# Kernel tuning notes

Measured on AMD Instinct MI355X. Metric: run time of the kernel, lower is better.

Reference implementation:

```python
import jax, jax.numpy as jnp
import numpy as np

G = 8           # graphs
NBG = 1024      # blocks per graph
APB = 4         # atoms per block
NC = 1          # coord channels
HID = 512
ES = 64
K = 9
L = 3
NLVL = 50
NB = G * NBG
NU = NB * APB
NUM_BLOCK, NUM_ATOM, NUM_POS = 25, 16, 16
BIG = 1e9


def _cumsum_ids(seg_lengths, n):
    # faithful to torch: zeros, mark segment starts via cumsum(lengths)[:-1], cumsum
    ids = jnp.zeros((n,), jnp.int32).at[jnp.cumsum(seg_lengths)[:-1]].set(1)
    return jnp.cumsum(ids)


def setup_inputs() -> dict:
    key = jax.random.key(0)
    ks = jax.random.split(key, 18)
    s = 0.02
    return {
        'Z': 3.0 * jax.random.normal(ks[0], (NU, NC, 3), jnp.float32),
        'B': jax.random.randint(ks[1], (NB,), 0, NUM_BLOCK),
        'A': jax.random.randint(ks[2], (NU,), 0, NUM_ATOM),
        'atom_positions': jax.random.randint(ks[3], (NU,), 0, NUM_POS),
        'block_lengths': jnp.full((NB,), APB, jnp.int32),
        'lengths': jnp.full((G,), NBG, jnp.int32),
        'segment_ids': jax.random.randint(ks[4], (NB,), 0, 2),
        'noise': jax.random.normal(ks[5], (NU, NC, 3), jnp.float32),
        'noise_level': jax.random.randint(ks[6], (G,), 0, NLVL),
        'sigmas': jnp.asarray(np.exp(np.linspace(np.log(10.0), np.log(0.01), NLVL)), jnp.float32),
        'atom_emb': s * jax.random.normal(ks[7], (NUM_ATOM, HID), jnp.float32),
        'pos_emb': s * jax.random.normal(ks[8], (NUM_POS, HID), jnp.float32),
        'block_emb': s * jax.random.normal(ks[9], (NUM_BLOCK, HID), jnp.float32),
        'edge_emb': s * jax.random.normal(ks[10], (2, ES), jnp.float32),
        'Wm': s * jax.random.normal(ks[11], (L, HID, HID), jnp.float32),
        'We': s * jax.random.normal(ks[12], (L, ES, HID), jnp.float32),
        'Wu': s * jax.random.normal(ks[13], (L, HID, HID), jnp.float32),
        'wz': s * jax.random.normal(ks[14], (L, HID), jnp.float32),
        'W1': s * jax.random.normal(ks[15], (HID, HID), jnp.float32),
        'b1': jnp.zeros((HID,), jnp.float32),
        'W2': s * jax.random.normal(ks[16], (HID, 1), jnp.float32),
    }


def _forward(Z, B, A, atom_positions, block_lengths, lengths, segment_ids,
             noise, noise_level, sigmas, atom_emb, pos_emb, block_emb, edge_emb,
             Wm, We, Wu, wz, W1, b1, W2):
    nb, nu, g = B.shape[0], A.shape[0], lengths.shape[0]
    nbg, apb = nb // g, nu // nb
    batch_id = _cumsum_ids(lengths, nb)        # [Nb]
    block_id = _cumsum_ids(block_lengths, nu)  # [Nu]

    # perturb: Z + noise * sigma[noise_level[graph]]
    used = sigmas[noise_level][batch_id][block_id]          # [Nu]
    Zp = Z + noise * used[:, None, None]                    # [Nu, NC, 3]

    # block embedding: atom + position + block-type
    H0 = atom_emb[A] + pos_emb[atom_positions] + block_emb[B][block_id]  # [Nu, H]

    # edges: fully connect -> split intra/inter by segment -> knn by min atom-pair distance
    xa = Zp.reshape(g, nbg * apb * NC, 3)
    sq = jnp.sum(xa * xa, axis=-1)
    d2 = sq[:, :, None] + sq[:, None, :] - 2.0 * jnp.einsum('gnd,gmd->gnm', xa, xa)
    D = d2.reshape(g, nbg, apb * NC, nbg, apb * NC).min(axis=(2, 4))     # [g, nbg, nbg]
    seg = segment_ids.reshape(g, nbg)
    same = seg[:, :, None] == seg[:, None, :]
    eye = jnp.eye(nbg, dtype=bool)[None]
    _, idx_intra = jax.lax.top_k(-jnp.where(same & ~eye, D, BIG), K)     # [g, nbg, K]
    _, idx_inter = jax.lax.top_k(-jnp.where(~same, D, BIG), K)
    off = (jnp.arange(g, dtype=jnp.int32) * nbg)[:, None, None]
    dst_loc = jnp.broadcast_to(jnp.arange(nbg, dtype=jnp.int32)[None, :, None] + off, (g, nbg, K))
    src = jnp.concatenate([(idx_intra + off).reshape(-1), (idx_inter + off).reshape(-1)])
    dst = jnp.concatenate([dst_loc.reshape(-1), dst_loc.reshape(-1)])
    eattr = edge_emb[jnp.concatenate([jnp.zeros(g * nbg * K, jnp.int32), jnp.ones(g * nbg * K, jnp.int32)])]

    # encoder (GET surrogate): block-level equivariant message passing
    h = jax.ops.segment_sum(H0, block_id, num_segments=nb) / apb                    # [Nb, H]
    Zb0 = jax.ops.segment_sum(Zp.mean(axis=1), block_id, num_segments=nb) / apb    # [Nb, 3]
    Zb = Zb0
    for l in range(Wm.shape[0]):
        m = jax.nn.silu((h[src] + h[dst]) @ Wm[l] + eattr @ We[l])                  # [E, H]
        h = h + jax.nn.silu(jax.ops.segment_sum(m, dst, num_segments=nb) @ Wu[l])
        coef = jnp.tanh(m @ wz[l])                                                  # [E]
        Zb = Zb + jax.ops.segment_sum((Zb[src] - Zb[dst]) * coef[:, None], dst, num_segments=nb) / (2 * K)
    pred_Z = Zp + (Zb - Zb0)[block_id][:, None, :]
    unit_repr = H0 + h[block_id]
    block_repr = h
    graph_repr = jax.ops.segment_sum(h, batch_id, num_segments=g)

    # energy head: SiLU -> Linear -> SiLU -> Linear(no bias), summed per graph
    e = jax.nn.silu(jax.nn.silu(block_repr) @ W1 + b1) @ W2                         # [Nb, 1]
    pred_energy = jax.ops.segment_sum(e[:, 0], batch_id, num_segments=g)            # [g]

    pred_noise = pred_Z - Zp
    per_unit = jnp.sum((pred_noise - noise) ** 2, axis=(-1, -2))                    # [Nu]
    nl = jax.ops.segment_sum(per_unit, batch_id[block_id], num_segments=g)
    loss = 0.5 * nl.mean()
    return pred_energy, pred_noise, unit_repr, block_repr, graph_repr, loss


def reference(Z, B, A, atom_positions, block_lengths, lengths, segment_ids,
              noise, noise_level, sigmas, atom_emb, pos_emb, block_emb, edge_emb,
              Wm, We, Wu, wz, W1, b1, W2):
    return _forward(Z, B, A, atom_positions, block_lengths, lengths, segment_ids,
                    noise, noise_level, sigmas, atom_emb, pos_emb, block_emb, edge_emb,
                    Wm, We, Wu, wz, W1, b1, W2)
```

## Files before the change

kernel.cpp:

```cpp
#include <hip/hip_runtime.h>
#include <hip/hip_bf16.h>

typedef __bf16 bf16;
typedef __bf16 bf16x2 __attribute__((ext_vector_type(2)));
typedef __bf16 bf16x8 __attribute__((ext_vector_type(8)));
typedef float floatx4 __attribute__((ext_vector_type(4)));

#define NB_ 8192
#define NU_ 32768

__device__ __forceinline__ float silu_f(float x) {
    float e = __expf(-x);
    return x * __builtin_amdgcn_rcpf(1.0f + e);
}

__device__ __forceinline__ float2 unpack_bf2(unsigned v) {
    float2 r;
    r.x = __uint_as_float(v << 16);
    r.y = __uint_as_float(v & 0xFFFF0000u);
    return r;
}

__device__ __forceinline__ void gll16(const bf16* g, bf16* l) {
    __builtin_amdgcn_global_load_lds((const __attribute__((address_space(1))) void*)g,
                                     (__attribute__((address_space(3))) void*)l, 16, 0, 0);
}

__global__ __launch_bounds__(256) void init_kernel(
    const float* __restrict__ Z, const float* __restrict__ noise,
    const int* __restrict__ nl, const float* __restrict__ sig,
    const int* __restrict__ Aarr, const int* __restrict__ posa, const int* __restrict__ Barr,
    const float* __restrict__ atom_emb, const float* __restrict__ pos_emb,
    const float* __restrict__ block_emb,
    const float* __restrict__ edge_emb, const float* __restrict__ We,
    const float* __restrict__ Wm, const float* __restrict__ Wu, const float* __restrict__ W1,
    float* __restrict__ Zp, float* __restrict__ Zb0, float* __restrict__ Zb,
    float* __restrict__ hf, bf16* __restrict__ hb,
    bf16* __restrict__ WmT, bf16* __restrict__ WuT, bf16* __restrict__ W1T,
    float* __restrict__ ebias,
    float* __restrict__ out_gr, float* __restrict__ out_e, float* __restrict__ out_loss)
{
    __shared__ float zsh[12];
    __shared__ float tile[32][33];
    int bid = blockIdx.x, tid = threadIdx.x;
    if (bid < 8192) {
        int b = bid, g = b >> 10;
        if (tid < 12) {
            float sg = sig[nl[g]];
            int idx = b*12 + tid;
            float zp = Z[idx] + noise[idx]*sg;
            Zp[idx] = zp;
            zsh[tid] = zp;
        }
        __syncthreads();
        if (tid < 3) {
            float v = 0.25f*(zsh[tid] + zsh[3+tid] + zsh[6+tid] + zsh[9+tid]);
            Zb0[b*3+tid] = v; Zb[b*3+tid] = v;
        }
        int ai[4], pi[4];
        #pragma unroll
        for (int a = 0; a < 4; a++) { ai[a] = Aarr[b*4+a]*512; pi[a] = posa[b*4+a]*512; }
        int bb = Barr[b]*512;
        #pragma unroll
        for (int cc = 0; cc < 2; cc++) {
            int c = tid + cc*256;
            float s = 0.0f;
            #pragma unroll
            for (int a = 0; a < 4; a++) s += atom_emb[ai[a]+c] + pos_emb[pi[a]+c];
            s = 0.25f*s + block_emb[bb+c];
            hf[(size_t)b*512+c] = s;
            hb[(size_t)b*512+c] = (bf16)s;
        }
        return;
    }
    bid -= 8192;
    if (bid < 1792) {
        int z = bid >> 8, rem = bid & 255;
        int bx = rem & 15, by = rem >> 4;
        int tx = tid & 31, ty = tid >> 5;
        const float* src; bf16* dst;
        if (z < 3)      { src = Wm + (size_t)z*262144;     dst = WmT + (size_t)z*262144; }
        else if (z < 6) { src = Wu + (size_t)(z-3)*262144; dst = WuT + (size_t)(z-3)*262144; }
        else            { src = W1;                        dst = W1T; }
        #pragma unroll
        for (int i = 0; i < 32; i += 8)
            tile[ty+i][tx] = src[(size_t)(by*32+ty+i)*512 + bx*32+tx];
        __syncthreads();
        #pragma unroll
        for (int i = 0; i < 32; i += 8)
            dst[(size_t)(bx*32+ty+i)*512 + by*32+tx] = (bf16)tile[tx][ty+i];
        return;
    }
    bid -= 1792;
    if (bid < 12) {
        int gid = bid*256 + tid;
        int l = gid >> 10, t = (gid >> 9) & 1, c = gid & 511;
        float s = 0.0f;
        #pragma unroll 8
        for (int e = 0; e < 64; e++)
            s += edge_emb[t*64 + e] * We[(size_t)(l*64 + e)*512 + c];
        ebias[gid] = s;
        return;
    }
    bid -= 12;
    int k = bid*256 + tid;
    if (k < 4096) out_gr[k] = 0.0f;
    else if (k < 4104) out_e[k-4096] = 0.0f;
    else if (k == 4104) out_loss[0] = 0.0f;
}

__device__ void knn_body(int kb, const float* __restrict__ Zp, const int* __restrict__ seg,
                         int* __restrict__ nbr) {
    int wid = threadIdx.x >> 6;
    int lane = threadIdx.x & 63;
    int r = ((kb & 7) << 10) + ((kb >> 3) << 2) + wid;
    int g = r >> 10;
    int il = r & 1023;
    int base = g << 10;
    int segr = seg[r];
    float za[4][3];
    #pragma unroll
    for (int a = 0; a < 4; a++)
        #pragma unroll
        for (int d = 0; d < 3; d++)
            za[a][d] = Zp[r*12 + a*3 + d];
    float dist[16];
    unsigned smask = 0;
    #pragma unroll
    for (int t = 0; t < 16; t++) {
        int jb = base + t*64 + lane;
        const float4* p = (const float4*)(Zp + (size_t)jb*12);
        float4 v0 = p[0], v1 = p[1], v2 = p[2];
        float bx[4] = {v0.x, v0.w, v1.z, v2.y};
        float by[4] = {v0.y, v1.x, v1.w, v2.z};
        float bz[4] = {v0.z, v1.y, v2.x, v2.w};
        float dm = 3.0e38f;
        #pragma unroll
        for (int a = 0; a < 4; a++) {
            #pragma unroll
            for (int bq = 0; bq < 4; bq++) {
                float dx = za[a][0]-bx[bq], dy = za[a][1]-by[bq], dz = za[a][2]-bz[bq];
                dm = fminf(dm, dx*dx + dy*dy + dz*dz);
            }
        }
        dist[t] = dm;
        if (seg[jb] == segr) smask |= (1u << t);
    }
    const float INF = 3.0e38f;
    for (int phase = 0; phase < 2; phase++) {
        float wd[16];
        #pragma unroll
        for (int t = 0; t < 16; t++) {
            bool ok = (phase == 0) ? (((smask >> t) & 1u) && (t*64 + lane != il))
                                   : (!((smask >> t) & 1u));
            wd[t] = ok ? dist[t] : INF;
        }
        for (int it = 0; it < 9; it++) {
            float bd = wd[0]; int bt = 0;
            #pragma unroll
            for (int t = 1; t < 16; t++) { if (wd[t] < bd) { bd = wd[t]; bt = t; } }
            float mv = bd;
            #pragma unroll
            for (int off = 32; off >= 1; off >>= 1) mv = fminf(mv, __shfl_xor(mv, off, 64));
            unsigned long long msk = __ballot(bd == mv);
            int wl = __ffsll(msk) - 1;
            int wt = __shfl(bt, wl, 64);
            if (lane == 0) nbr[r*18 + phase*9 + it] = base + wt*64 + wl;
            bool amwin = (lane == wl);
            #pragma unroll
            for (int t = 0; t < 16; t++) if (amwin && t == wt) wd[t] = INF;
        }
    }
}

template<int PIPE>
__device__ void gemm_body(const bf16* __restrict__ A, const bf16* __restrict__ BT,
                          bf16* __restrict__ Pb, float* __restrict__ hf,
                          bf16* __restrict__ hb, bf16* __restrict__ shp,
                          const float* __restrict__ b1, const float* __restrict__ W2,
                          float* __restrict__ out_e,
                          float* __restrict__ Zb, const float* __restrict__ zacc,
                          int mode, int bid)
{
    constexpr int NBUF = PIPE ? 3 : 1;
    __shared__ alignas(16) bf16 sA[NBUF*128*32];
    __shared__ alignas(16) bf16 sB[NBUF*64*32];
    int mt = bid & 63, nt = bid >> 6;
    int m0 = mt*128, n0 = nt*64;
    int tid = threadIdx.x, lane = tid & 63, w = tid >> 6;
    int wm = w & 1, wn = w >> 1;
    int lm = lane & 15, q = lane >> 4;

    int pA0 = w*128 + lane, pA1 = pA0 + 64, pB = w*64 + lane;
    int rA0 = pA0 >> 2, qA0 = (pA0 & 3) ^ ((rA0 >> 1) & 3);
    int rA1 = pA1 >> 2, qA1 = (pA1 & 3) ^ ((rA1 >> 1) & 3);
    int rB  = pB  >> 2, qB  = (pB  & 3) ^ ((rB  >> 1) & 3);
    const bf16* gA0 = A  + (size_t)(m0 + rA0)*512 + qA0*8;
    const bf16* gA1 = A  + (size_t)(m0 + rA1)*512 + qA1*8;
    const bf16* gB  = BT + (size_t)(n0 + rB )*512 + qB*8;
    int dA0 = (w*128)*8, dA1 = (w*128 + 64)*8, dB = (w*64)*8;

    int swq = (q ^ ((lm >> 1) & 3)) * 8;
    int offA[4], offB[2];
    #pragma unroll
    for (int tm = 0; tm < 4; tm++) offA[tm] = (wm*64 + tm*16 + lm)*32 + swq;
    #pragma unroll
    for (int tn = 0; tn < 2; tn++) offB[tn] = (wn*32 + tn*16 + lm)*32 + swq;

    floatx4 zv = {0.0f, 0.0f, 0.0f, 0.0f};
    floatx4 acc[4][2];
    #pragma unroll
    for (int i = 0; i < 4; i++)
        #pragma unroll
        for (int j = 0; j < 2; j++) acc[i][j] = zv;

    if constexpr (PIPE == 0) {
        for (int k0 = 0; k0 < 512; k0 += 32) {
            gll16(gA0 + k0, sA + dA0);
            gll16(gA1 + k0, sA + dA1);
            gll16(gB  + k0, sB + dB);
            __syncthreads();
            bf16x8 af[4], bfr[2];
            #pragma unroll
            for (int tm = 0; tm < 4; tm++) af[tm] = *(const bf16x8*)(sA + offA[tm]);
            #pragma unroll
            for (int tn = 0; tn < 2; tn++) bfr[tn] = *(const bf16x8*)(sB + offB[tn]);
            #pragma unroll
            for (int tm = 0; tm < 4; tm++)
                #pragma unroll
                for (int tn = 0; tn < 2; tn++)
                    acc[tm][tn] = __builtin_amdgcn_mfma_f32_16x16x32_bf16(af[tm], bfr[tn], acc[tm][tn], 0, 0, 0);
            __syncthreads();
        }
    } else {
        gll16(gA0,      sA + dA0);
        gll16(gA1,      sA + dA1);
        gll16(gB,       sB + dB);
        gll16(gA0 + 32, sA + 4096 + dA0);
        gll16(gA1 + 32, sA + 4096 + dA1);
        gll16(gB  + 32, sB + 2048 + dB);
        #pragma unroll
        for (int t = 0; t < 16; t++) {
            const int cur = t % 3;
            if (t < 14) {
                const int k0 = (t + 2) * 32;
                const int nb = (t + 2) % 3;
                gll16(gA0 + k0, sA + nb*4096 + dA0);
                gll16(gA1 + k0, sA + nb*4096 + dA1);
                gll16(gB  + k0, sB + nb*2048 + dB);
                asm volatile("s_waitcnt vmcnt(6)" ::: "memory");
            } else if (t == 14) {
                asm volatile("s_waitcnt vmcnt(3)" ::: "memory");
            } else {
                asm volatile("s_waitcnt vmcnt(0)" ::: "memory");
            }
            __builtin_amdgcn_s_barrier();
            asm volatile("" ::: "memory");
            const bf16* a_ = sA + cur*4096;
            const bf16* b_ = sB + cur*2048;
            bf16x8 af[4], bfr[2];
            #pragma unroll
            for (int tm = 0; tm < 4; tm++) af[tm] = *(const bf16x8*)(a_ + offA[tm]);
            #pragma unroll
            for (int tn = 0; tn < 2; tn++) bfr[tn] = *(const bf16x8*)(b_ + offB[tn]);
            #pragma unroll
            for (int tm = 0; tm < 4; tm++)
                #pragma unroll
                for (int tn = 0; tn < 2; tn++)
                    acc[tm][tn] = __builtin_amdgcn_mfma_f32_16x16x32_bf16(af[tm], bfr[tn], acc[tm][tn], 0, 0, 0);
            asm volatile("" ::: "memory");
            __builtin_amdgcn_s_barrier();
        }
    }

    if (mode == 1 && nt == 0) {
        int o = m0*3 + tid;
        Zb[o] += zacc[o] * (1.0f/18.0f);
        if (tid < 128) {
            int o2 = m0*3 + 256 + tid;
            Zb[o2] += zacc[o2] * (1.0f/18.0f);
        }
    }

    if (mode == 2) {
        float esum = 0.0f;
        #pragma unroll
        for (int tn = 0; tn < 2; tn++) {
            int col = n0 + wn*32 + tn*16 + lm;
            float bb = b1[col];
            float w2 = W2[col];
            #pragma unroll
            for (int tm = 0; tm < 4; tm++)
                #pragma unroll
                for (int rr = 0; rr < 4; rr++)
                    esum += silu_f(acc[tm][tn][rr] + bb) * w2;
        }
        #pragma unroll
        for (int off = 32; off >= 1; off >>= 1) esum += __shfl_xor(esum, off, 64);
        __shared__ float ered[4];
        if (lane == 0) ered[w] = esum;
        __syncthreads();
        if (tid == 0) {
            float tot = ered[0] + ered[1] + ered[2] + ered[3];
            atomicAdd(&out_e[m0 >> 10], tot);
        }
        return;
    }
    #pragma unroll
    for (int tm = 0; tm < 4; tm++) {
        #pragma unroll
        for (int tn = 0; tn < 2; tn++) {
            #pragma unroll
            for (int rr = 0; rr < 4; rr++) {
                int row = m0 + wm*64 + tm*16 + q*4 + rr;
                int col = n0 + wn*32 + tn*16 + lm;
                size_t o = (size_t)row*512 + col;
                float v = acc[tm][tn][rr];
                if (mode == 0) {
                    Pb[o] = (bf16)v;
                } else {
                    float nh = hf[o] + silu_f(v);
                    hf[o] = nh;
                    hb[o] = (bf16)nh;
                    if (shp) shp[o] = (bf16)silu_f(nh);
                }
            }
        }
    }
}

__global__ __launch_bounds__(256) void gemm_kernel(const bf16* __restrict__ A, const bf16* __restrict__ BT,
                                                   bf16* __restrict__ Pb, float* __restrict__ hf,
                                                   bf16* __restrict__ hb, bf16* __restrict__ shp,
                                                   const float* __restrict__ b1, const float* __restrict__ W2,
                                                   float* __restrict__ out_e,
                                                   float* __restrict__ Zb, const float* __restrict__ zacc,
                                                   int mode) {
    gemm_body<1>(A, BT, Pb, hf, hb, shp, b1, W2, out_e, Zb, zacc, mode, blockIdx.x);
}

__global__ __launch_bounds__(256) void knn_pgemm0_kernel(const bf16* __restrict__ hb,
                                                         const bf16* __restrict__ WmT0,
                                                         bf16* __restrict__ Pb,
                                                         const float* __restrict__ Zp,
                                                         const int* __restrict__ seg,
                                                         int* __restrict__ nbr) {
    if (blockIdx.x < 512)
        gemm_body<0>(hb, WmT0, Pb, nullptr, nullptr, nullptr, nullptr, nullptr, nullptr,
                     nullptr, nullptr, 0, blockIdx.x);
    else
        knn_body(blockIdx.x - 512, Zp, seg, nbr);
}

__global__ __launch_bounds__(256) void edge_kernel(const bf16* __restrict__ Pb, const float* __restrict__ ebias,
                                                   const float* __restrict__ wz, const float* __restrict__ Zb,
                                                   const int* __restrict__ nbr, bf16* __restrict__ msum,
                                                   float* __restrict__ zacc) {
    int bid = blockIdx.x, tid = threadIdx.x;
    int b = ((bid & 7) << 10) | (bid >> 3);
    int c0 = 2*tid;
    int lane = tid & 63, wid = tid >> 6;
    __shared__ int srcs[18];
    __shared__ float red[18][4];
    __shared__ float term[18][3];
    if (tid < 18) srcs[tid] = nbr[b*18 + tid];
    __syncthreads();
    float2 pd  = unpack_bf2(*(const unsigned*)(Pb + (size_t)b*512 + c0));
    float2 eb0 = *(const float2*)(ebias + c0);
    float2 eb1 = *(const float2*)(ebias + 512 + c0);
    float2 w   = *(const float2*)(wz + c0);
    float ms0 = 0.0f, ms1 = 0.0f;
    float pdot[18];
    #pragma unroll
    for (int e = 0; e < 18; e++) {
        int s = srcs[e];
        float2 pv = unpack_bf2(*(const unsigned*)(Pb + (size_t)s*512 + c0));
        float ba = (e < 9) ? eb0.x : eb1.x;
        float bb = (e < 9) ? eb0.y : eb1.y;
        float m0 = silu_f(pv.x + pd.x + ba);
        float m1 = silu_f(pv.y + pd.y + bb);
        ms0 += m0; ms1 += m1;
        pdot[e] = m0*w.x + m1*w.y;
    }
    bf16x2 mp = { (bf16)ms0, (bf16)ms1 };
    *(bf16x2*)(msum + (size_t)b*512 + c0) = mp;
    #pragma unroll
    for (int e = 0; e < 18; e++) {
        float v = pdot[e];
        #pragma unroll
        for (int off = 32; off >= 1; off >>= 1) v += __shfl_xor(v, off, 64);
        if (lane == 0) red[e][wid] = v;
    }
    __syncthreads();
    if (tid < 18) {
        float dot = red[tid][0] + red[tid][1] + red[tid][2] + red[tid][3];
        float coef = tanhf(dot);
        int s = srcs[tid];
        #pragma unroll
        for (int d = 0; d < 3; d++)
            term[tid][d] = (Zb[s*3 + d] - Zb[b*3 + d]) * coef;
    }
    __syncthreads();
    if (tid < 3) {
        float s = 0.0f;
        #pragma unroll
        for (int e = 0; e < 18; e++) s += term[e][tid];
        zacc[b*3 + tid] = s;
    }
}

__global__ __launch_bounds__(256) void finalize_kernel(const float* __restrict__ hf, float* __restrict__ out_gr,
                                                       const float* __restrict__ Zb, const float* __restrict__ Zb0,
                                                       const float* __restrict__ noise,
                                                       float* __restrict__ out_pn, float* __restrict__ out_loss) {
    __shared__ float red[256];
    int bid = blockIdx.x, tid = threadIdx.x;
    if (bid < 128) {
        int u = bid*256 + tid;
        int b = u >> 2;
        float per = 0.0f;
        #pragma unroll
        for (int d = 0; d < 3; d++) {
            float dv = Zb[b*3+d] - Zb0[b*3+d];
            out_pn[u*3+d] = dv;
            float e = dv - noise[u*3+d];
            per += e*e;
        }
        red[tid] = per; __syncthreads();
        for (int st = 128; st > 0; st >>= 1) {
            if (tid < st) red[tid] += red[tid+st];
            __syncthreads();
        }
        if (tid == 0) atomicAdd(out_loss, red[0] * (1.0f/16.0f));
        return;
    }
    int pid = bid - 128;
    int g = pid >> 5;
    int rc = (pid >> 1) & 15;
    int ch = pid & 1;
    int c = ch*256 + tid;
    int b0 = (g << 10) + rc*64;
    float s = 0.0f;
    for (int i = 0; i < 64; i++) s += hf[(size_t)(b0+i)*512 + c];
    atomicAdd(&out_gr[g*512 + c], s);
}

__global__ __launch_bounds__(256) void unitrepr_kernel(const int* __restrict__ Aarr, const int* __restrict__ posa,
                                                       const int* __restrict__ Barr,
                                                       const float* __restrict__ atom_emb, const float* __restrict__ pos_emb,
                                                       const float* __restrict__ block_emb,
                                                       const float* __restrict__ hf, float* __restrict__ out_ur) {
    int gid = blockIdx.x*256 + threadIdx.x;
    int u = gid >> 7, c = (gid & 127) << 2, b = u >> 2;
    float4 va = *(const float4*)(atom_emb + (size_t)Aarr[u]*512 + c);
    float4 vp = *(const float4*)(pos_emb + (size_t)posa[u]*512 + c);
    float4 vb = *(const float4*)(block_emb + (size_t)Barr[b]*512 + c);
    float4 vh = *(const float4*)(hf + (size_t)b*512 + c);
    float4 o;
    o.x = va.x + vp.x + vb.x + vh.x;
    o.y = va.y + vp.y + vb.y + vh.y;
    o.z = va.z + vp.z + vb.z + vh.z;
    o.w = va.w + vp.w + vb.w + vh.w;
    *(float4*)(out_ur + (size_t)u*512 + c) = o;
}

extern "C" void kernel_launch(void* const* d_in, const int* in_sizes, int n_in,
                              void* d_out, int out_size, void* d_ws, size_t ws_size,
                              hipStream_t stream) {
    const float* Z         = (const float*)d_in[0];
    const int*   B         = (const int*)d_in[1];
    const int*   A         = (const int*)d_in[2];
    const int*   ap        = (const int*)d_in[3];
    const int*   seg       = (const int*)d_in[6];
    const float* noise     = (const float*)d_in[7];
    const int*   nl        = (const int*)d_in[8];
    const float* sig       = (const float*)d_in[9];
    const float* atom_emb  = (const float*)d_in[10];
    const float* pos_emb   = (const float*)d_in[11];
    const float* block_emb = (const float*)d_in[12];
    const float* edge_emb  = (const float*)d_in[13];
    const float* Wm        = (const float*)d_in[14];
    const float* We        = (const float*)d_in[15];
    const float* Wu        = (const float*)d_in[16];
    const float* wz        = (const float*)d_in[17];
    const float* W1        = (const float*)d_in[18];
    const float* b1        = (const float*)d_in[19];
    const float* W2        = (const float*)d_in[20];
    (void)in_sizes; (void)n_in; (void)d_ws; (void)ws_size; (void)out_size;

    float* out = (float*)d_out;
    const size_t o1 = 8, o2 = 98312, o3 = 16875528, o4 = 21069832, o5 = 21073928;
    float* out_e    = out;
    float* out_pn   = out + o1;
    float* out_ur   = out + o2;
    float* hf       = out + o3;
    float* out_gr   = out + o4;
    float* out_loss = out + o5;

    char* arena = (char*)(out + o2);
    bf16*  Pb   = (bf16*)(arena);
    bf16*  msum = (bf16*)(arena + 16777216);
    bf16*  sh   = (bf16*)(arena + 25165824);
    bf16*  hb   = (bf16*)(arena + 33554432);
    float* Zp   = (float*)(arena + 41943040);
    float* Zb0  = (float*)(arena + 42336256);
    float* Zb   = (float*)(arena + 42434560);
    float* zacc = (float*)(arena + 42532864);
    int*   nbr  = (int*)  (arena + 42631168);
    bf16*  WmT  = (bf16*) (arena + 43220992);
    bf16*  WuT  = (bf16*) (arena + 44793856);
    bf16*  W1T  = (bf16*) (arena + 46366720);
    float* ebias= (float*)(arena + 46891008);

    init_kernel<<<8192 + 1792 + 12 + 17, 256, 0, stream>>>(
        Z, noise, nl, sig, A, ap, B, atom_emb, pos_emb, block_emb,
        edge_emb, We, Wm, Wu, W1,
        Zp, Zb0, Zb, hf, hb, WmT, WuT, W1T, ebias, out_gr, out_e, out_loss);

    knn_pgemm0_kernel<<<512 + 2048, 256, 0, stream>>>(hb, WmT, Pb, Zp, seg, nbr);

    for (int l = 0; l < 3; l++) {
        if (l > 0)
            gemm_kernel<<<512, 256, 0, stream>>>(hb, WmT + (size_t)l*262144, Pb,
                                                 nullptr, nullptr, nullptr, nullptr, nullptr, nullptr,
                                                 nullptr, nullptr, 0);
        edge_kernel<<<8192, 256, 0, stream>>>(Pb, ebias + l*1024, wz + l*512, Zb, nbr, msum, zacc);
        gemm_kernel<<<512, 256, 0, stream>>>(msum, WuT + (size_t)l*262144, nullptr,
                                             hf, hb, (l == 2) ? sh : nullptr, nullptr, nullptr, nullptr,
                                             Zb, zacc, 1);
    }
    gemm_kernel<<<512, 256, 0, stream>>>(sh, W1T, nullptr, nullptr, nullptr, nullptr,
                                         b1, W2, out_e, nullptr, nullptr, 2);
    finalize_kernel<<<384, 256, 0, stream>>>(hf, out_gr, Zb, Zb0, noise, out_pn, out_loss);
    unitrepr_kernel<<<16384, 256, 0, stream>>>(A, ap, B, atom_emb, pos_emb, block_emb, hf, out_ur);
}
```

Baseline: 482.8 us.

## Fuse finalize into last update GEMM and move weight prep into kNN launch

```diff
diff --git a/kernel.cpp b/kernel.cpp
--- a/kernel.cpp
+++ b/kernel.cpp
@@ -5,9 +5,7 @@
 typedef __bf16 bf16x2 __attribute__((ext_vector_type(2)));
 typedef __bf16 bf16x8 __attribute__((ext_vector_type(8)));
 typedef float floatx4 __attribute__((ext_vector_type(4)));
-
-#define NB_ 8192
-#define NU_ 32768
+typedef float floatx2 __attribute__((ext_vector_type(2)));
 
 __device__ __forceinline__ float silu_f(float x) {
     float e = __expf(-x);
@@ -32,13 +30,10 @@
     const int* __restrict__ Aarr, const int* __restrict__ posa, const int* __restrict__ Barr,
     const float* __restrict__ atom_emb, const float* __restrict__ pos_emb,
     const float* __restrict__ block_emb,
-    const float* __restrict__ edge_emb, const float* __restrict__ We,
-    const float* __restrict__ Wm, const float* __restrict__ Wu, const float* __restrict__ W1,
+    const float* __restrict__ Wm,
     float* __restrict__ Zp, float* __restrict__ Zb0, float* __restrict__ Zb,
     float* __restrict__ hf, bf16* __restrict__ hb,
-    bf16* __restrict__ WmT, bf16* __restrict__ WuT, bf16* __restrict__ W1T,
-    float* __restrict__ ebias,
-    float* __restrict__ out_gr, float* __restrict__ out_e, float* __restrict__ out_loss)
+    bf16* __restrict__ WmT)
 {
     __shared__ float zsh[12];
     __shared__ float tile[32][33];
@@ -73,40 +68,16 @@
         }
         return;
     }
-    bid -= 8192;
-    if (bid < 1792) {
-        int z = bid >> 8, rem = bid & 255;
-        int bx = rem & 15, by = rem >> 4;
-        int tx = tid & 31, ty = tid >> 5;
-        const float* src; bf16* dst;
-        if (z < 3)      { src = Wm + (size_t)z*262144;     dst = WmT + (size_t)z*262144; }
-        else if (z < 6) { src = Wu + (size_t)(z-3)*262144; dst = WuT + (size_t)(z-3)*262144; }
-        else            { src = W1;                        dst = W1T; }
-        #pragma unroll
-        for (int i = 0; i < 32; i += 8)
-            tile[ty+i][tx] = src[(size_t)(by*32+ty+i)*512 + bx*32+tx];
-        __syncthreads();
-        #pragma unroll
-        for (int i = 0; i < 32; i += 8)
-            dst[(size_t)(bx*32+ty+i)*512 + by*32+tx] = (bf16)tile[tx][ty+i];
-        return;
-    }
-    bid -= 1792;
-    if (bid < 12) {
-        int gid = bid*256 + tid;
-        int l = gid >> 10, t = (gid >> 9) & 1, c = gid & 511;
-        float s = 0.0f;
-        #pragma unroll 8
-        for (int e = 0; e < 64; e++)
-            s += edge_emb[t*64 + e] * We[(size_t)(l*64 + e)*512 + c];
-        ebias[gid] = s;
-        return;
-    }
-    bid -= 12;
-    int k = bid*256 + tid;
-    if (k < 4096) out_gr[k] = 0.0f;
-    else if (k < 4104) out_e[k-4096] = 0.0f;
-    else if (k == 4104) out_loss[0] = 0.0f;
+    int rem = bid - 8192;
+    int bx = rem & 15, by = rem >> 4;
+    int tx = tid & 31, ty = tid >> 5;
+    #pragma unroll
+    for (int i = 0; i < 32; i += 8)
+        tile[ty+i][tx] = Wm[(size_t)(by*32+ty+i)*512 + bx*32+tx];
+    __syncthreads();
+    #pragma unroll
+    for (int i = 0; i < 32; i += 8)
+        WmT[(size_t)(bx*32+ty+i)*512 + by*32+tx] = (bf16)tile[tx][ty+i];
 }
 
 __device__ void knn_body(int kb, const float* __restrict__ Zp, const int* __restrict__ seg,
@@ -124,6 +95,13 @@
         #pragma unroll
         for (int d = 0; d < 3; d++)
             za[a][d] = Zp[r*12 + a*3 + d];
+    floatx2 ax[4], ay[4], az[4];
+    #pragma unroll
+    for (int a = 0; a < 4; a++) {
+        ax[a] = (floatx2){za[a][0], za[a][0]};
+        ay[a] = (floatx2){za[a][1], za[a][1]};
+        az[a] = (floatx2){za[a][2], za[a][2]};
+    }
     float dist[16];
     unsigned smask = 0;
     #pragma unroll
@@ -131,19 +109,19 @@
         int jb = base + t*64 + lane;
         const float4* p = (const float4*)(Zp + (size_t)jb*12);
         float4 v0 = p[0], v1 = p[1], v2 = p[2];
-        float bx[4] = {v0.x, v0.w, v1.z, v2.y};
-        float by[4] = {v0.y, v1.x, v1.w, v2.z};
-        float bz[4] = {v0.z, v1.y, v2.x, v2.w};
-        float dm = 3.0e38f;
+        floatx2 bx0 = {v0.x, v0.w}, by0 = {v0.y, v1.x}, bz0 = {v0.z, v1.y};
+        floatx2 bx1 = {v1.z, v2.y}, by1 = {v1.w, v2.z}, bz1 = {v2.x, v2.w};
+        floatx2 mn = {3.0e38f, 3.0e38f};
         #pragma unroll
         for (int a = 0; a < 4; a++) {
-            #pragma unroll
-            for (int bq = 0; bq < 4; bq++) {
-                float dx = za[a][0]-bx[bq], dy = za[a][1]-by[bq], dz = za[a][2]-bz[bq];
-                dm = fminf(dm, dx*dx + dy*dy + dz*dz);
-            }
-        }
-        dist[t] = dm;
+            floatx2 dx = ax[a] - bx0, dy = ay[a] - by0, dz = az[a] - bz0;
+            floatx2 dd = dx*dx + dy*dy + dz*dz;
+            mn.x = fminf(mn.x, dd.x); mn.y = fminf(mn.y, dd.y);
+            dx = ax[a] - bx1; dy = ay[a] - by1; dz = az[a] - bz1;
+            dd = dx*dx + dy*dy + dz*dz;
+            mn.x = fminf(mn.x, dd.x); mn.y = fminf(mn.y, dd.y);
+        }
+        dist[t] = fminf(mn.x, mn.y);
         if (seg[jb] == segr) smask |= (1u << t);
     }
     const float INF = 3.0e38f;
@@ -180,11 +158,17 @@
                           const float* __restrict__ b1, const float* __restrict__ W2,
                           float* __restrict__ out_e,
                           float* __restrict__ Zb, const float* __restrict__ zacc,
+                          const float* __restrict__ Zb0, const float* __restrict__ noise,
+                          float* __restrict__ out_pn, float* __restrict__ out_loss,
+                          float* __restrict__ out_gr,
                           int mode, int bid)
 {
     constexpr int NBUF = PIPE ? 3 : 1;
     __shared__ alignas(16) bf16 sA[NBUF*128*32];
     __shared__ alignas(16) bf16 sB[NBUF*64*32];
+    __shared__ float grbuf[4][32];
+    __shared__ float lsh[4];
+    __shared__ float ered[4];
     int mt = bid & 63, nt = bid >> 6;
     int m0 = mt*128, n0 = nt*64;
     int tid = threadIdx.x, lane = tid & 63, w = tid >> 6;
@@ -297,7 +281,6 @@
         }
         #pragma unroll
         for (int off = 32; off >= 1; off >>= 1) esum += __shfl_xor(esum, off, 64);
-        __shared__ float ered[4];
         if (lane == 0) ered[w] = esum;
         __syncthreads();
         if (tid == 0) {
@@ -306,6 +289,8 @@
         }
         return;
     }
+
+    float colsum[2] = {0.0f, 0.0f};
     #pragma unroll
     for (int tm = 0; tm < 4; tm++) {
         #pragma unroll
@@ -321,10 +306,48 @@
                 } else {
                     float nh = hf[o] + silu_f(v);
                     hf[o] = nh;
-                    hb[o] = (bf16)nh;
+                    colsum[tn] += nh;
                     if (shp) shp[o] = (bf16)silu_f(nh);
+                    else     hb[o] = (bf16)nh;
                 }
             }
+        }
+    }
+
+    if (mode == 1 && shp) {
+        #pragma unroll
+        for (int tn = 0; tn < 2; tn++) {
+            float v = colsum[tn];
+            v += __shfl_xor(v, 16, 64);
+            v += __shfl_xor(v, 32, 64);
+            if (q == 0) grbuf[w][tn*16 + lm] = v;
+        }
+        __syncthreads();
+        if (((w & 1) == 0) && lane < 32) {
+            float tot = grbuf[w][lane] + grbuf[w + 1][lane];
+            int col = n0 + (w >> 1)*32 + lane;
+            atomicAdd(&out_gr[(m0 >> 10)*512 + col], tot);
+        }
+        if (nt == 0) {
+            float per2 = 0.0f;
+            #pragma unroll
+            for (int j = 0; j < 2; j++) {
+                int u = m0*4 + tid*2 + j;
+                int b = u >> 2;
+                #pragma unroll
+                for (int d = 0; d < 3; d++) {
+                    float dv = Zb[b*3 + d] - Zb0[b*3 + d];
+                    out_pn[(size_t)u*3 + d] = dv;
+                    float e = dv - noise[(size_t)u*3 + d];
+                    per2 += e*e;
+                }
+            }
+            #pragma unroll
+            for (int off = 32; off >= 1; off >>= 1) per2 += __shfl_xor(per2, off, 64);
+            if (lane == 0) lsh[w] = per2;
+            __syncthreads();
+            if (tid == 0)
+                atomicAdd(out_loss, (lsh[0]+lsh[1]+lsh[2]+lsh[3]) * (1.0f/16.0f));
         }
     }
 }
@@ -335,21 +358,77 @@
                                                    const float* __restrict__ b1, const float* __restrict__ W2,
                                                    float* __restrict__ out_e,
                                                    float* __restrict__ Zb, const float* __restrict__ zacc,
+                                                   const float* __restrict__ Zb0, const float* __restrict__ noise,
+                                                   float* __restrict__ out_pn, float* __restrict__ out_loss,
+                                                   float* __restrict__ out_gr,
                                                    int mode) {
-    gemm_body<1>(A, BT, Pb, hf, hb, shp, b1, W2, out_e, Zb, zacc, mode, blockIdx.x);
+    gemm_body<1>(A, BT, Pb, hf, hb, shp, b1, W2, out_e, Zb, zacc,
+                 Zb0, noise, out_pn, out_loss, out_gr, mode, blockIdx.x);
 }
 
 __global__ __launch_bounds__(256) void knn_pgemm0_kernel(const bf16* __restrict__ hb,
-                                                         const bf16* __restrict__ WmT0,
+                                                         const bf16* __restrict__ WmT,
                                                          bf16* __restrict__ Pb,
                                                          const float* __restrict__ Zp,
                                                          const int* __restrict__ seg,
-                                                         int* __restrict__ nbr) {
-    if (blockIdx.x < 512)
-        gemm_body<0>(hb, WmT0, Pb, nullptr, nullptr, nullptr, nullptr, nullptr, nullptr,
-                     nullptr, nullptr, 0, blockIdx.x);
-    else
-        knn_body(blockIdx.x - 512, Zp, seg, nbr);
+                                                         int* __restrict__ nbr,
+                                                         const float* __restrict__ Wm,
+                                                         const float* __restrict__ Wu,
+                                                         const float* __restrict__ W1,
+                                                         bf16* __restrict__ WmTw,
+                                                         bf16* __restrict__ WuT,
+                                                         bf16* __restrict__ W1T,
+                                                         const float* __restrict__ edge_emb,
+                                                         const float* __restrict__ We,
+                                                         float* __restrict__ ebias,
+                                                         float* __restrict__ out_gr,
+                                                         float* __restrict__ out_e,
+                                                         float* __restrict__ out_loss) {
+    __shared__ float ttile[32][33];
+    int bid = blockIdx.x, tid = threadIdx.x;
+    if (bid < 512) {
+        gemm_body<0>(hb, WmT, Pb, nullptr, nullptr, nullptr, nullptr, nullptr, nullptr,
+                     nullptr, nullptr, nullptr, nullptr, nullptr, nullptr, nullptr, 0, bid);
+        return;
+    }
+    if (bid < 2560) {
+        knn_body(bid - 512, Zp, seg, nbr);
+        return;
+    }
+    int tb = bid - 2560;
+    if (tb < 1536) {
+        int z = 1 + (tb >> 8), rem = tb & 255;
+        int bx = rem & 15, by = rem >> 4;
+        int tx = tid & 31, ty = tid >> 5;
+        const float* src; bf16* dst;
+        if (z < 3)      { src = Wm + (size_t)z*262144;     dst = WmTw + (size_t)z*262144; }
+        else if (z < 6) { src = Wu + (size_t)(z-3)*262144; dst = WuT + (size_t)(z-3)*262144; }
+        else            { src = W1;                        dst = W1T; }
+        #pragma unroll
+        for (int i = 0; i < 32; i += 8)
+            ttile[ty+i][tx] = src[(size_t)(by*32+ty+i)*512 + bx*32+tx];
+        __syncthreads();
+        #pragma unroll
+        for (int i = 0; i < 32; i += 8)
+            dst[(size_t)(bx*32+ty+i)*512 + by*32+tx] = (bf16)ttile[tx][ty+i];
+        return;
+    }
+    tb -= 1536;
+    if (tb < 12) {
+        int gid = tb*256 + tid;
+        int l = gid >> 10, t = (gid >> 9) & 1, c = gid & 511;
+        float s = 0.0f;
+        #pragma unroll 8
+        for (int e = 0; e < 64; e++)
+            s += edge_emb[t*64 + e] * We[(size_t)(l*64 + e)*512 + c];
+        ebias[gid] = s;
+        return;
+    }
+    tb -= 12;
+    int k = tb*256 + tid;
+    if (k < 4096) out_gr[k] = 0.0f;
+    else if (k < 4104) out_e[k-4096] = 0.0f;
+    else if (k == 4104) out_loss[0] = 0.0f;
 }
 
 __global__ __launch_bounds__(256) void edge_kernel(const bf16* __restrict__ Pb, const float* __restrict__ ebias,
@@ -407,42 +486,6 @@
         for (int e = 0; e < 18; e++) s += term[e][tid];
         zacc[b*3 + tid] = s;
     }
-}
-
-__global__ __launch_bounds__(256) void finalize_kernel(const float* __restrict__ hf, float* __restrict__ out_gr,
-                                                       const float* __restrict__ Zb, const float* __restrict__ Zb0,
-                                                       const float* __restrict__ noise,
-                                                       float* __restrict__ out_pn, float* __restrict__ out_loss) {
-    __shared__ float red[256];
-    int bid = blockIdx.x, tid = threadIdx.x;
-    if (bid < 128) {
-        int u = bid*256 + tid;
-        int b = u >> 2;
-        float per = 0.0f;
-        #pragma unroll
-        for (int d = 0; d < 3; d++) {
-            float dv = Zb[b*3+d] - Zb0[b*3+d];
-            out_pn[u*3+d] = dv;
-            float e = dv - noise[u*3+d];
-            per += e*e;
-        }
-        red[tid] = per; __syncthreads();
-        for (int st = 128; st > 0; st >>= 1) {
-            if (tid < st) red[tid] += red[tid+st];
-            __syncthreads();
-        }
-        if (tid == 0) atomicAdd(out_loss, red[0] * (1.0f/16.0f));
-        return;
-    }
-    int pid = bid - 128;
-    int g = pid >> 5;
-    int rc = (pid >> 1) & 15;
-    int ch = pid & 1;
-    int c = ch*256 + tid;
-    int b0 = (g << 10) + rc*64;
-    float s = 0.0f;
-    for (int i = 0; i < 64; i++) s += hf[(size_t)(b0+i)*512 + c];
-    atomicAdd(&out_gr[g*512 + c], s);
 }
 
 __global__ __launch_bounds__(256) void unitrepr_kernel(const int* __restrict__ Aarr, const int* __restrict__ posa,
@@ -512,25 +555,27 @@
     bf16*  W1T  = (bf16*) (arena + 46366720);
     float* ebias= (float*)(arena + 46891008);
 
-    init_kernel<<<8192 + 1792 + 12 + 17, 256, 0, stream>>>(
+    init_kernel<<<8192 + 256, 256, 0, stream>>>(
         Z, noise, nl, sig, A, ap, B, atom_emb, pos_emb, block_emb,
-        edge_emb, We, Wm, Wu, W1,
-        Zp, Zb0, Zb, hf, hb, WmT, WuT, W1T, ebias, out_gr, out_e, out_loss);
-
-    knn_pgemm0_kernel<<<512 + 2048, 256, 0, stream>>>(hb, WmT, Pb, Zp, seg, nbr);
+        Wm, Zp, Zb0, Zb, hf, hb, WmT);
+
+    knn_pgemm0_kernel<<<512 + 2048 + 1536 + 12 + 17, 256, 0, stream>>>(
+        hb, WmT, Pb, Zp, seg, nbr,
+        Wm, Wu, W1, WmT, WuT, W1T,
+        edge_emb, We, ebias, out_gr, out_e, out_loss);
 
     for (int l = 0; l < 3; l++) {
         if (l > 0)
             gemm_kernel<<<512, 256, 0, stream>>>(hb, WmT + (size_t)l*262144, Pb,
                                                  nullptr, nullptr, nullptr, nullptr, nullptr, nullptr,
-                                                 nullptr, nullptr, 0);
+                                                 nullptr, nullptr, nullptr, nullptr, nullptr, nullptr, nullptr, 0);
         edge_kernel<<<8192, 256, 0, stream>>>(Pb, ebias + l*1024, wz + l*512, Zb, nbr, msum, zacc);
         gemm_kernel<<<512, 256, 0, stream>>>(msum, WuT + (size_t)l*262144, nullptr,
                                              hf, hb, (l == 2) ? sh : nullptr, nullptr, nullptr, nullptr,
-                                             Zb, zacc, 1);
+                                             Zb, zacc, Zb0, noise, out_pn, out_loss, out_gr, 1);
     }
     gemm_kernel<<<512, 256, 0, stream>>>(sh, W1T, nullptr, nullptr, nullptr, nullptr,
-                                         b1, W2, out_e, nullptr, nullptr, 2);
-    finalize_kernel<<<384, 256, 0, stream>>>(hf, out_gr, Zb, Zb0, noise, out_pn, out_loss);
+                                         b1, W2, out_e, nullptr, nullptr,
+                                         nullptr, nullptr, nullptr, nullptr, nullptr, 2);
     unitrepr_kernel<<<16384, 256, 0, stream>>>(A, ap, B, atom_emb, pos_emb, block_emb, hf, out_ur);
 }
```

After: 472.5 us. 1.02x faster.
